# Performance work log

Measured on AMD Instinct MI355X. Metric: run time of the kernel, lower is better.

The kernel has to match this reference:

```python
import jax, jax.numpy as jnp
import numpy as np

B, IN_CH, OUT_CH, L = 8, 64, 64, 2048
LUT = 256  # uint8 value range


def setup_inputs() -> dict:
    key = jax.random.key(0)
    k1, k2 = jax.random.split(key)
    # pre-transpose input: [B, in_channels, out_channels, L], values are uint8-range indices
    x = jax.random.randint(k1, (B, IN_CH, OUT_CH, L), 0, LUT, dtype=jnp.int32)
    # per-(out_channel, in_channel) lookup table of 256 entries
    white_table = jax.random.uniform(k2, (OUT_CH, IN_CH, LUT), dtype=jnp.float32)
    return {"x": x, "white_table": white_table}


def reference(x, white_table):
    # transpose(dim0=1, dim1=2): [B, in, out, L] -> [B, out, in, L]
    xt = jnp.swapaxes(x, 1, 2)
    O, I, _ = white_table.shape
    oi = jnp.arange(O)[None, :, None, None]  # broadcast over batch/L
    ii = jnp.arange(I)[None, None, :, None]
    # fused per-(i,j) LUT gather: out[b,i,j,l] = white_table[i, j, xt[b,i,j,l]]
    return white_table[oi, ii, xt]
```

## Files before the change

### kernel.cpp

```cpp
#include <hip/hip_runtime.h>


#define BATCH  8
#define IN_CH  64
#define OUT_CH 64
#define LEN    2048
#define LUTN   256

__global__ __launch_bounds__(256) void WhiteTranspose_28406913696445_kernel(
    const int* __restrict__ x,
    const float* __restrict__ table,
    float* __restrict__ out)
{
    __shared__ float lut[LUTN];

    const int row = blockIdx.x;
    const int i = row & (IN_CH - 1);
    const int o = (row >> 6) & (OUT_CH - 1);
    const int b = row >> 12;

    lut[threadIdx.x] = table[(o * IN_CH + i) * LUTN + threadIdx.x];
    __syncthreads();

    const int4* __restrict__ xin =
        (const int4*)(x + ((size_t)((b * IN_CH + i) * OUT_CH + o) * LEN));
    float4* __restrict__ dst =
        (float4*)(out + ((size_t)row * LEN));

    #pragma unroll
    for (int it = 0; it < 2; ++it) {
        const int idx = threadIdx.x + it * 256;
        const int4 v = xin[idx];
        float4 r;
        r.x = lut[v.x];
        r.y = lut[v.y];
        r.z = lut[v.z];
        r.w = lut[v.w];
        dst[idx] = r;
    }
}

extern "C" void kernel_launch(void* const* d_in, const int* in_sizes, int n_in,
                              void* d_out, int out_size, void* d_ws, size_t ws_size,
                              hipStream_t stream) {
    const int*   x     = (const int*)d_in[0];
    const float* table = (const float*)d_in[1];
    float*       out   = (float*)d_out;

    const int n_rows = BATCH * OUT_CH * IN_CH;
    WhiteTranspose_28406913696445_kernel<<<n_rows, 256, 0, stream>>>(x, table, out);
}
```

Baseline: 430.7 us.

## Reuse each LUT across all batches per block and use nontemporal loads/stores

Each block now handles one (out, in) table pair and loops over all 8 batches, so each 1 KB LUT is loaded into shared memory once instead of eight times. The grid shrinks from 32768 to 4096 blocks, and each block does eight times more streaming work with 16 independent vector loads in flight. Global loads and stores are made nontemporal to avoid cache pollution on this purely streaming workload. Fewer blocks may reduce latency hiding, but 4096 blocks still fills the device.

```diff
diff --git a/kernel.cpp b/kernel.cpp
--- a/kernel.cpp
+++ b/kernel.cpp
@@ -7,6 +7,9 @@
 #define LEN    2048
 #define LUTN   256
 
+typedef int   i32x4 __attribute__((ext_vector_type(4)));
+typedef float f32x4 __attribute__((ext_vector_type(4)));
+
 __global__ __launch_bounds__(256) void WhiteTranspose_28406913696445_kernel(
     const int* __restrict__ x,
     const float* __restrict__ table,
@@ -14,29 +17,35 @@
 {
     __shared__ float lut[LUTN];
 
-    const int row = blockIdx.x;
-    const int i = row & (IN_CH - 1);
-    const int o = (row >> 6) & (OUT_CH - 1);
-    const int b = row >> 12;
+    const int pair = blockIdx.x;
+    const int i = pair & (IN_CH - 1);
+    const int o = pair >> 6;
 
-    lut[threadIdx.x] = table[(o * IN_CH + i) * LUTN + threadIdx.x];
+    lut[threadIdx.x] = table[(size_t)pair * LUTN + threadIdx.x];
     __syncthreads();
 
-    const int4* __restrict__ xin =
-        (const int4*)(x + ((size_t)((b * IN_CH + i) * OUT_CH + o) * LEN));
-    float4* __restrict__ dst =
-        (float4*)(out + ((size_t)row * LEN));
+    const size_t x_row0      = (size_t)(i * OUT_CH + o) * LEN;
+    const size_t out_row0    = (size_t)(o * IN_CH + i) * LEN;
+    const size_t x_bstride   = (size_t)IN_CH * OUT_CH * LEN;
+    const size_t out_bstride = (size_t)OUT_CH * IN_CH * LEN;
 
     #pragma unroll
-    for (int it = 0; it < 2; ++it) {
-        const int idx = threadIdx.x + it * 256;
-        const int4 v = xin[idx];
-        float4 r;
-        r.x = lut[v.x];
-        r.y = lut[v.y];
-        r.z = lut[v.z];
-        r.w = lut[v.w];
-        dst[idx] = r;
+    for (int b = 0; b < BATCH; ++b) {
+        const i32x4* __restrict__ xin =
+            (const i32x4*)(x + x_row0 + (size_t)b * x_bstride);
+        f32x4* __restrict__ dst =
+            (f32x4*)(out + out_row0 + (size_t)b * out_bstride);
+        #pragma unroll
+        for (int it = 0; it < 2; ++it) {
+            const int idx = threadIdx.x + it * 256;
+            const i32x4 v = __builtin_nontemporal_load(&xin[idx]);
+            f32x4 r;
+            r.x = lut[v.x];
+            r.y = lut[v.y];
+            r.z = lut[v.z];
+            r.w = lut[v.w];
+            __builtin_nontemporal_store(r, &dst[idx]);
+        }
     }
 }
 
@@ -47,6 +56,6 @@
     const float* table = (const float*)d_in[1];
     float*       out   = (float*)d_out;
 
-    const int n_rows = BATCH * OUT_CH * IN_CH;
-    WhiteTranspose_28406913696445_kernel<<<n_rows, 256, 0, stream>>>(x, table, out);
+    const int n_pairs = OUT_CH * IN_CH;
+    WhiteTranspose_28406913696445_kernel<<<n_pairs, 256, 0, stream>>>(x, table, out);
 }
```

Result: no change. 426.1 us (-1.1%).
